# Performance work log

Measured on AMD Instinct MI355X. Metric: run time of the kernel, lower is better.

Reference implementation:

```python
import jax, jax.numpy as jnp
import numpy as np
from math import pi

H = 1024        # hidden_size
CAP = 32        # capacity (even -> CAP//2 even+odd rotation pairs)
EH = H // 2         # even_hidden_size = 512
OH = (H - 1) // 2   # odd_hidden_size  = 511
PAIRS = CAP // 2    # 16

# fixed permutations (hidden_size even branch of the original module)
_PE = np.arange(H).reshape(-1, 2)[:, ::-1].reshape(-1)                       # swap (0,1),(2,3),...
_inner = np.arange(1, 2 * OH + 1).reshape(-1, 2)[:, ::-1].reshape(-1)
_PO = np.concatenate([[0], _inner, [2 * OH + 1]])                            # fix ends, swap interior pairs


def cm(x, y):
    """complex multiply; real/imag stacked in last dim."""
    xr, xi = x[..., 0], x[..., 1]
    yr, yi = y[..., 0], y[..., 1]
    return jnp.stack([xr * yr - xi * yi, xr * yi + xi * yr], -1)


def _ilv(a, b):
    """interleave two [n] vectors -> [2n]."""
    return jnp.stack([a, b], 1).reshape(-1)


def setup_inputs() -> dict:
    key = jax.random.key(0)
    ks = jax.random.split(key, 6)
    u = lambda k, shape: jax.random.uniform(k, shape, jnp.float32) * (2 * pi) - pi
    return {
        "x": jax.random.normal(ks[0], (4096, H, 2), jnp.float32),
        "omega": u(ks[1], (H,)),
        "even_theta": u(ks[2], (PAIRS, EH)),
        "odd_theta": u(ks[3], (PAIRS, OH)),
        "even_phi": u(ks[4], (PAIRS, EH)),
        "odd_phi": u(ks[5], (PAIRS, OH)),
    }


def reference(x, omega, even_theta, odd_theta, even_phi, odd_phi):
    PE = jnp.asarray(_PE)
    PO = jnp.asarray(_PO)

    def step(xc, p):
        et, ep, ot, op = p
        # ---- even rotation (note: original code swaps cos_phi/sin_phi in the
        # call to _v_diag/_v_off_diag; replicated faithfully here) ----
        ct, st, cp, sp = jnp.cos(et), jnp.sin(et), jnp.cos(ep), jnp.sin(ep)
        z = jnp.zeros_like(ct)
        vd = jnp.stack([_ilv(sp * ct, ct), _ilv(cp * ct, z)], -1)          # [H,2]
        vo = jnp.stack([_ilv(-sp * st, st), _ilv(-cp * st, z)], -1)        # [H,2]
        xc = cm(xc, vd) + cm(xc[:, PE, :], vo)
        # ---- odd rotation (ends padded with identity) ----
        ct, st, cp, sp = jnp.cos(ot), jnp.sin(ot), jnp.cos(op), jnp.sin(op)
        z = jnp.zeros_like(ct)
        one = jnp.ones((1,), xc.dtype)
        zero = jnp.zeros((1,), xc.dtype)
        vd_re = jnp.concatenate([one, _ilv(sp * ct, ct), one])
        vd_im = jnp.concatenate([zero, _ilv(cp * ct, z), zero])
        vo_re = jnp.concatenate([zero, _ilv(-sp * st, st), zero])
        vo_im = jnp.concatenate([zero, _ilv(-cp * st, z), zero])
        xc = cm(xc, jnp.stack([vd_re, vd_im], -1)) + cm(xc[:, PO, :], jnp.stack([vo_re, vo_im], -1))
        return xc, None

    x, _ = jax.lax.scan(step, x, (even_theta, even_phi, odd_theta, odd_phi))
    # final diagonal phase
    x = cm(x, jnp.stack([jnp.cos(omega), jnp.sin(omega)], -1))
    return x
```

## Files before the change

### kernel.cpp

```cpp
#include <hip/hip_runtime.h>
#include <math.h>


typedef float f4 __attribute__((ext_vector_type(4)));
typedef float f2 __attribute__((ext_vector_type(2)));

#define OMCS_OFF 65536

__device__ __forceinline__ f2 rot_t(f2 c, f2 A, f2 B) {
  f2 m, t;
  asm("v_pk_mul_f32 %0, %1, %2 op_sel:[1,0] op_sel_hi:[1,1]"
      : "=v"(m) : "v"(c), "v"(B));
  asm("v_pk_fma_f32 %0, %1, %2, %3 op_sel:[0,0,0] op_sel_hi:[0,1,1] "
      "neg_lo:[0,0,1] neg_hi:[0,0,1]"
      : "=v"(t) : "v"(c), "v"(A), "v"(m));
  return t;
}
__device__ __forceinline__ f2 rot_d(f2 c, f2 T) {
  f2 a, d;
  asm("v_pk_mul_f32 %0, %1, %2 op_sel:[1,0] op_sel_hi:[0,0]"
      : "=v"(a) : "v"(c), "v"(T));
  asm("v_pk_fma_f32 %0, %1, %2, %3 op_sel:[0,1,0] op_sel_hi:[1,1,1] "
      "neg_lo:[1,0,0] neg_hi:[0,0,0]"
      : "=v"(d) : "v"(c), "v"(T), "v"(a));
  return d;
}
__device__ __forceinline__ f2 rot_o(f2 c, f2 A, f2 B) {
  f2 m, o;
  asm("v_pk_mul_f32 %0, %1, %2 op_sel:[0,0] op_sel_hi:[0,1]"
      : "=v"(m) : "v"(c), "v"(B));
  asm("v_pk_fma_f32 %0, %1, %2, %3 op_sel:[1,0,0] op_sel_hi:[1,1,1]"
      : "=v"(o) : "v"(c), "v"(A), "v"(m));
  return o;
}
__device__ __forceinline__ f2 cmulp(f2 W, f2 V) {
  f2 m, o;
  asm("v_pk_mul_f32 %0, %1, %2 op_sel:[1,1] op_sel_hi:[1,0]"
      : "=v"(m) : "v"(W), "v"(V));
  asm("v_pk_fma_f32 %0, %1, %2, %3 op_sel:[0,0,0] op_sel_hi:[0,1,1] "
      "neg_lo:[0,0,1] neg_hi:[0,0,0]"
      : "=v"(o) : "v"(W), "v"(V), "v"(m));
  return o;
}

__global__ __launch_bounds__(256) void eunn_precompute(
    const float* __restrict__ omega, const float* __restrict__ et,
    const float* __restrict__ ot, const float* __restrict__ ep,
    const float* __restrict__ op, float* __restrict__ ws) {
  int tid = blockIdx.x * 256 + threadIdx.x;
  if (tid < 16384) {
    int s = tid >> 10, k = tid & 1023;
    int phase = k >> 9, j = k & 511;
    float ct, st, cp, sp;
    if (phase == 0) {
      sincosf(et[s * 512 + j], &st, &ct);
      sincosf(ep[s * 512 + j], &sp, &cp);
    } else if (j < 511) {
      sincosf(ot[s * 511 + j], &st, &ct);
      sincosf(op[s * 511 + j], &sp, &cp);
    } else {
      ct = 1.f; st = 0.f; cp = 0.f; sp = 1.f;
    }
    ((f4*)ws)[s * 1024 + phase * 512 + (j & 7) * 64 + (j >> 3)] =
        (f4){ct, st, cp, sp};
  } else if (tid < 16896) {
    int m = tid - 16384;
    float s0, c0, s1, c1;
    sincosf(omega[2 * m], &s0, &c0);
    sincosf(omega[2 * m + 1], &s1, &c1);
    ((f4*)(ws + OMCS_OFF))[(m & 7) * 64 + (m >> 3)] = (f4){c0, s0, c1, s1};
  }
}

template <int R>
__global__ __launch_bounds__(256, 2) void eunn_main(
    const float* __restrict__ x, float* __restrict__ out,
    const float* __restrict__ ws) {
  const int lane = threadIdx.x & 63;
  const int wid = blockIdx.x * (blockDim.x >> 6) + (threadIdx.x >> 6);
  const f4* cf = (const f4*)ws + lane;

  f2 ea[R][8], eb[R][8];
#pragma unroll
  for (int r = 0; r < R; ++r) {
    const f4* xr = (const f4*)(x + (size_t)(wid * R + r) * 2048) + lane * 8;
#pragma unroll
    for (int p = 0; p < 8; ++p) {
      f4 t = xr[p];
      ea[r][p] = (f2){t.x, t.y};
      eb[r][p] = (f2){t.z, t.w};
    }
  }

  f4 E[8];
#pragma unroll
  for (int p = 0; p < 8; ++p) E[p] = cf[p * 64];

#pragma unroll 1
  for (int s = 0; s < 16; ++s) {
    f4 O[8];
    {
      const f4* ob = cf + s * 1024 + 512;
#pragma unroll
      for (int p = 0; p < 8; ++p) O[p] = ob[p * 64];
    }
#pragma unroll
    for (int r = 0; r < R; ++r) {
#pragma unroll
      for (int p = 0; p < 8; ++p) {
        f2 cxy = (f2){E[p].x, E[p].y};
        f2 czw = (f2){E[p].z, E[p].w};
        f2 a = ea[r][p], b = eb[r][p];
        f2 T = rot_t(cxy, a, b);
        ea[r][p] = rot_d(czw, T);
        eb[r][p] = rot_o(cxy, a, b);
      }
    }
    {
      const f4* nb = cf + ((s + 1) & 15) * 1024;
#pragma unroll
      for (int p = 0; p < 8; ++p) E[p] = nb[p * 64];
    }
    {
      float ctm = __shfl_up(O[7].x, 1, 64);
      float stm = __shfl_up(O[7].y, 1, 64);
      if (lane == 0) { ctm = 1.f; stm = 0.f; }
      f2 cm2 = (f2){ctm, stm};
#pragma unroll
      for (int r = 0; r < R; ++r) {
        float upx = __shfl_down(ea[r][0].x, 1, 64);
        float upy = __shfl_down(ea[r][0].y, 1, 64);
        float dnz = __shfl_up(eb[r][7].x, 1, 64);
        float dnw = __shfl_up(eb[r][7].y, 1, 64);
        f2 D = (f2){dnz, dnw};
        ea[r][0] = rot_o(cm2, D, ea[r][0]);
#pragma unroll
        for (int p = 0; p < 7; ++p) {
          f2 oxy = (f2){O[p].x, O[p].y};
          f2 ozw = (f2){O[p].z, O[p].w};
          f2 A = eb[r][p], B = ea[r][p + 1];
          f2 T = rot_t(oxy, A, B);
          eb[r][p] = rot_d(ozw, T);
          ea[r][p + 1] = rot_o(oxy, A, B);
        }
        {
          f2 oxy = (f2){O[7].x, O[7].y};
          f2 ozw = (f2){O[7].z, O[7].w};
          f2 UP = (f2){upx, upy};
          f2 T = rot_t(oxy, eb[r][7], UP);
          eb[r][7] = rot_d(ozw, T);
        }
      }
    }
  }

  const f4* om4 = (const f4*)(ws + OMCS_OFF) + lane;
#pragma unroll
  for (int r = 0; r < R; ++r) {
    f4* outr = (f4*)(out + (size_t)(wid * R + r) * 2048) + lane * 8;
#pragma unroll
    for (int p = 0; p < 8; ++p) {
      f4 w = om4[p * 64];
      f2 o1 = cmulp((f2){w.x, w.y}, ea[r][p]);
      f2 o2 = cmulp((f2){w.z, w.w}, eb[r][p]);
      outr[p] = (f4){o1.x, o1.y, o2.x, o2.y};
    }
  }
}

extern "C" void kernel_launch(void* const* d_in, const int* in_sizes, int n_in,
                              void* d_out, int out_size, void* d_ws, size_t ws_size,
                              hipStream_t stream) {
  const float* x     = (const float*)d_in[0];
  const float* omega = (const float*)d_in[1];
  const float* et    = (const float*)d_in[2];
  const float* ot    = (const float*)d_in[3];
  const float* ep    = (const float*)d_in[4];
  const float* op    = (const float*)d_in[5];
  float* out = (float*)d_out;
  float* ws  = (float*)d_ws;

  eunn_precompute<<<dim3(66), dim3(256), 0, stream>>>(omega, et, ot, ep, op, ws);

  eunn_main<2><<<dim3(512), dim3(256), 0, stream>>>(x, out, ws);
}
```

Measured before the change: 116.6 us.

## Stage per-step rotation coefficients in double-buffered LDS shared across block

Each step's coefficients are now loaded cooperatively by all 256 threads into a double-buffered shared-memory tile, instead of every wavefront loading all 16 float4 values itself from global memory. The next step's coefficients are fetched into registers at the top of the loop and written to LDS at the end, followed by a block barrier. This cuts redundant global and L2 traffic per wave, at the cost of 32 KB of LDS, a __syncthreads per step, and extra registers for the prefetch.

```diff
diff --git a/kernel.cpp b/kernel.cpp
--- a/kernel.cpp
+++ b/kernel.cpp
@@ -76,9 +76,13 @@
 __global__ __launch_bounds__(256, 2) void eunn_main(
     const float* __restrict__ x, float* __restrict__ out,
     const float* __restrict__ ws) {
-  const int lane = threadIdx.x & 63;
-  const int wid = blockIdx.x * (blockDim.x >> 6) + (threadIdx.x >> 6);
-  const f4* cf = (const f4*)ws + lane;
+  __shared__ f4 cbuf[2][1024];
+  const int tid = threadIdx.x;
+  const int lane = tid & 63;
+  const int wid = blockIdx.x * (blockDim.x >> 6) + (tid >> 6);
+  const f4* wsf = (const f4*)ws;
+
+  f4 p0 = wsf[tid], p1 = wsf[tid + 256], p2 = wsf[tid + 512], p3 = wsf[tid + 768];
 
   f2 ea[R][8], eb[R][8];
 #pragma unroll
@@ -92,18 +96,24 @@
     }
   }
 
-  f4 E[8];
-#pragma unroll
-  for (int p = 0; p < 8; ++p) E[p] = cf[p * 64];
+  cbuf[0][tid] = p0;
+  cbuf[0][tid + 256] = p1;
+  cbuf[0][tid + 512] = p2;
+  cbuf[0][tid + 768] = p3;
+  __syncthreads();
 
 #pragma unroll 1
   for (int s = 0; s < 16; ++s) {
-    f4 O[8];
-    {
-      const f4* ob = cf + s * 1024 + 512;
+    const int cur = s & 1, nxt = cur ^ 1;
+    const f4* nb = wsf + ((s + 1) & 15) * 1024;
+    f4 n0 = nb[tid], n1 = nb[tid + 256], n2 = nb[tid + 512], n3 = nb[tid + 768];
+
+    f4 E[8], O[8];
 #pragma unroll
-      for (int p = 0; p < 8; ++p) O[p] = ob[p * 64];
-    }
+    for (int p = 0; p < 8; ++p) E[p] = cbuf[cur][p * 64 + lane];
+#pragma unroll
+    for (int p = 0; p < 8; ++p) O[p] = cbuf[cur][512 + p * 64 + lane];
+
 #pragma unroll
     for (int r = 0; r < R; ++r) {
 #pragma unroll
@@ -116,11 +126,7 @@
         eb[r][p] = rot_o(cxy, a, b);
       }
     }
-    {
-      const f4* nb = cf + ((s + 1) & 15) * 1024;
-#pragma unroll
-      for (int p = 0; p < 8; ++p) E[p] = nb[p * 64];
-    }
+
     {
       float ctm = __shfl_up(O[7].x, 1, 64);
       float stm = __shfl_up(O[7].y, 1, 64);
@@ -152,6 +158,12 @@
         }
       }
     }
+
+    cbuf[nxt][tid] = n0;
+    cbuf[nxt][tid + 256] = n1;
+    cbuf[nxt][tid + 512] = n2;
+    cbuf[nxt][tid + 768] = n3;
+    __syncthreads();
   }
 
   const f4* om4 = (const f4*)(ws + OMCS_OFF) + lane;
```

New measurement: 119.6 us. 2.6% more time.
